# Optimization experiments

Measured on AMD Instinct MI355X. Metric: run time of the kernel, lower is better.

The kernel has to match this reference:

```python
import jax, jax.numpy as jnp
import numpy as np

SEQ_LENGTH = 256
MID_O = 800
OUT_DIM = 128

def _lstm_cell(x, h, c, Wih, Whh, bih, bhh):
    # PyTorch gate order: i, f, g, o
    gates = x @ Wih.T + h @ Whh.T + bih + bhh
    i, f, g, o = jnp.split(gates, 4, axis=-1)
    c = jax.nn.sigmoid(f) * c + jax.nn.sigmoid(i) * jnp.tanh(g)
    h = jax.nn.sigmoid(o) * jnp.tanh(c)
    return h, c

def _lstm_layer(x_seq, Wih, Whh, bih, bhh):
    B = x_seq.shape[1]
    H = Whh.shape[1]
    h0 = jnp.zeros((B, H), x_seq.dtype)
    c0 = jnp.zeros((B, H), x_seq.dtype)
    def step(carry, xt):
        h, c = carry
        h, c = _lstm_cell(xt, h, c, Wih, Whh, bih, bhh)
        return (h, c), h
    (hT, cT), out = jax.lax.scan(step, (h0, c0), x_seq)
    return out, hT, cT

def _lstm_params(key, in_dim, hid, scale=0.05):
    k1, k2, k3, k4 = jax.random.split(key, 4)
    return (jax.random.normal(k1, (4 * hid, in_dim), jnp.float32) * scale,
            jax.random.normal(k2, (4 * hid, hid), jnp.float32) * scale,
            jax.random.normal(k3, (4 * hid,), jnp.float32) * scale,
            jax.random.normal(k4, (4 * hid,), jnp.float32) * scale)

def setup_inputs() -> dict:
    key = jax.random.key(0)
    ks = jax.random.split(key, 10)
    input_dim, mid_i, latent, mid_o, out_dim = 128, 60, 20, MID_O, OUT_DIM
    x = jax.random.normal(ks[0], (SEQ_LENGTH, 1024, input_dim), jnp.float32)
    fc1 = _lstm_params(ks[1], input_dim, mid_i)
    fc21 = _lstm_params(ks[2], mid_i, latent)
    l3 = _lstm_params(ks[3], latent, latent)
    l4 = _lstm_params(ks[4], latent, mid_o)
    l5 = _lstm_params(ks[5], mid_o, out_dim)
    id_W = jax.random.normal(ks[6], (latent, latent), jnp.float32) * 0.05
    id_b = jnp.zeros((latent,), jnp.float32)
    down_W = jax.random.normal(ks[7], (latent, out_dim), jnp.float32) * 0.05
    down_b = jnp.zeros((latent,), jnp.float32)
    d = {"x": x,
         "fc1_Wih": fc1[0], "fc1_Whh": fc1[1], "fc1_bih": fc1[2], "fc1_bhh": fc1[3],
         "fc21_Wih": fc21[0], "fc21_Whh": fc21[1], "fc21_bih": fc21[2], "fc21_bhh": fc21[3],
         "l3_Wih": l3[0], "l3_Whh": l3[1], "l3_bih": l3[2], "l3_bhh": l3[3],
         "l4_Wih": l4[0], "l4_Whh": l4[1], "l4_bih": l4[2], "l4_bhh": l4[3],
         "l5_Wih": l5[0], "l5_Whh": l5[1], "l5_bih": l5[2], "l5_bhh": l5[3],
         "id_W": id_W, "id_b": id_b, "down_W": down_W, "down_b": down_b}
    return d

def reference(x, fc1_Wih, fc1_Whh, fc1_bih, fc1_bhh,
              fc21_Wih, fc21_Whh, fc21_bih, fc21_bhh,
              l3_Wih, l3_Whh, l3_bih, l3_bhh,
              l4_Wih, l4_Whh, l4_bih, l4_bhh,
              l5_Wih, l5_Whh, l5_bih, l5_bhh,
              id_W, id_b, down_W, down_b):
    # ---- encode ----
    out1, _, _ = _lstm_layer(x, fc1_Wih, fc1_Whh, fc1_bih, fc1_bhh)
    h1 = jax.nn.relu(out1)
    _, mu, c_mean = _lstm_layer(h1, fc21_Wih, fc21_Whh, fc21_bih, fc21_bhh)
    # ---- decode (deterministic: z = mu, c_t = cell_mean) ----
    B = mu.shape[0]
    output0 = mu @ id_W.T + id_b
    h2 = jnp.zeros((B, MID_O), x.dtype); c2 = jnp.zeros((B, MID_O), x.dtype)
    h3 = jnp.zeros((B, OUT_DIM), x.dtype); c3 = jnp.zeros((B, OUT_DIM), x.dtype)
    def step(carry, _):
        h, c, h2, c2, h3, c3, out = carry
        h, c = _lstm_cell(out, h, c, l3_Wih, l3_Whh, l3_bih, l3_bhh)
        h2, c2 = _lstm_cell(h, h2, c2, l4_Wih, l4_Whh, l4_bih, l4_bhh)
        h3, c3 = _lstm_cell(h2, h3, c3, l5_Wih, l5_Whh, l5_bih, l5_bhh)
        out = h3 @ down_W.T + down_b
        return (h, c, h2, c2, h3, c3, out), h3
    _, outMean = jax.lax.scan(step, (mu, c_mean, h2, c2, h3, c3, output0), None, length=SEQ_LENGTH)
    return outMean, mu
```

## Files before the change

kernel.cpp:

```cpp
#include <hip/hip_runtime.h>
#include <stdint.h>

typedef __bf16 bf16x8 __attribute__((ext_vector_type(8)));
typedef float  f32x4  __attribute__((ext_vector_type(4)));

static __device__ __forceinline__ unsigned short f2bf(float f) {
  unsigned int u = __float_as_uint(f);
  u = u + 0x7fffu + ((u >> 16) & 1u);
  return (unsigned short)(u >> 16);
}
static __device__ __forceinline__ float bf2f(unsigned short h) {
  return __uint_as_float(((unsigned int)h) << 16);
}
static __device__ __forceinline__ float sigm(float x) {
  return 1.f / (1.f + __expf(-x));
}
static __device__ __forceinline__ float tanh_f(float x) {
  float ax = fabsf(x);
  float e = __expf(-2.f * ax);
  float t = (1.f - e) / (1.f + e);
  return copysignf(t, x);
}

__global__ void kPrep(const float* __restrict__ w4i, const float* __restrict__ w4h,
                      const float* __restrict__ b4i, const float* __restrict__ b4h,
                      const float* __restrict__ w5i, const float* __restrict__ w5h,
                      const float* __restrict__ b5i, const float* __restrict__ b5h,
                      const float* __restrict__ w1i, const float* __restrict__ w1h,
                      const float* __restrict__ b1i, const float* __restrict__ b1h,
                      const float* __restrict__ w2i, const float* __restrict__ w2h,
                      const float* __restrict__ b2i, const float* __restrict__ b2h,
                      const float* __restrict__ w3i, const float* __restrict__ w3h,
                      const float* __restrict__ b3i, const float* __restrict__ b3h,
                      unsigned short* __restrict__ W4, unsigned short* __restrict__ W5,
                      float* __restrict__ W1, float* __restrict__ W2, float* __restrict__ W3,
                      float* __restrict__ b4, float* __restrict__ b5,
                      float* __restrict__ b1, float* __restrict__ b2, float* __restrict__ b3) {
  int idx0 = blockIdx.x * blockDim.x + threadIdx.x;
  int stride = gridDim.x * blockDim.x;
  const int TOT = 3197328;
  for (int i = idx0; i < TOT; i += stride) {
    int i2 = i;
    if (i2 < 2662400) {
      int n = i2 / 832, k = i2 % 832;
      float v = (k < 20) ? w4i[n * 20 + k]
                         : ((k >= 24 && k < 824) ? w4h[n * 800 + (k - 24)] : 0.f);
      W4[i2] = f2bf(v);
      continue;
    }
    i2 -= 2662400;
    if (i2 < 475136) {
      int n = i2 / 928, k = i2 % 928;
      float v = (k < 800) ? w5i[n * 800 + k] : w5h[n * 128 + (k - 800)];
      W5[i2] = f2bf(v);
      continue;
    }
    i2 -= 475136;
    if (i2 < 46080) {
      int n = i2 / 192, k = i2 % 192;
      W1[i2] = (k < 128) ? w1i[n * 128 + k] : ((k < 188) ? w1h[n * 60 + (k - 128)] : 0.f);
      continue;
    }
    i2 -= 46080;
    if (i2 < 6400) {
      int n = i2 / 80, k = i2 % 80;
      W2[i2] = (k < 60) ? w2i[n * 60 + k] : w2h[n * 20 + (k - 60)];
      continue;
    }
    i2 -= 6400;
    if (i2 < 3200) {
      int n = i2 / 40, k = i2 % 40;
      W3[i2] = (k < 20) ? w3i[n * 20 + k] : w3h[n * 20 + (k - 20)];
      continue;
    }
    i2 -= 3200;
    if (i2 < 3200) { b4[i2] = b4i[i2] + b4h[i2]; continue; }
    i2 -= 3200;
    if (i2 < 512) { b5[i2] = b5i[i2] + b5h[i2]; continue; }
    i2 -= 512;
    if (i2 < 240) { b1[i2] = b1i[i2] + b1h[i2]; continue; }
    i2 -= 240;
    if (i2 < 80) { b2[i2] = b2i[i2] + b2h[i2]; continue; }
    i2 -= 80;
    b3[i2] = b3i[i2] + b3h[i2];
  }
}

__global__ void kZero(float* __restrict__ c2, float* __restrict__ c3,
                      unsigned int* __restrict__ h2, unsigned int* __restrict__ h3) {
  int idx = blockIdx.x * blockDim.x + threadIdx.x;
  int stride = gridDim.x * blockDim.x;
  for (int i = idx; i < 819200; i += stride) c2[i] = 0.f;
  for (int i = idx; i < 131072; i += stride) c3[i] = 0.f;
  for (int i = idx; i < 409600; i += stride) h2[i] = 0u;
  for (int i = idx; i < 65536; i += stride) h3[i] = 0u;
}

__global__ __launch_bounds__(256, 2)
void kEnc(const float* __restrict__ x,
          const float* __restrict__ W1, const float* __restrict__ b1,
          const float* __restrict__ W2, const float* __restrict__ b2,
          const float* __restrict__ idW, const float* __restrict__ idb,
          float* __restrict__ hl30, float* __restrict__ cl30,
          float* __restrict__ out0, float* __restrict__ muOut) {
  __shared__ float xb[512];
  __shared__ float hb[240], cbb[240], h1b[240];
  __shared__ float h21[80], c21[80];
  __shared__ float g1[960], g2[320];
  const int tid = threadIdx.x;
  const int rowbase = blockIdx.x * 4;
  if (tid < 240) { hb[tid] = 0.f; cbb[tid] = 0.f; h1b[tid] = 0.f; }
  if (tid < 80) { h21[tid] = 0.f; c21[tid] = 0.f; }
  __syncthreads();
  for (int t = 0; t < 256; ++t) {
    const float* xs = x + ((size_t)t * 1024 + rowbase) * 128;
    xb[tid] = xs[tid];
    xb[tid + 256] = xs[tid + 256];
    __syncthreads();
    if (tid < 240) {
      const float* wr = W1 + tid * 192;
      float s0 = b1[tid], s1 = s0, s2 = s0, s3 = s0;
      for (int k = 0; k < 128; ++k) {
        float w = wr[k];
        s0 += w * xb[k]; s1 += w * xb[128 + k]; s2 += w * xb[256 + k]; s3 += w * xb[384 + k];
      }
      for (int k = 0; k < 60; ++k) {
        float w = wr[128 + k];
        s0 += w * hb[k]; s1 += w * hb[60 + k]; s2 += w * hb[120 + k]; s3 += w * hb[180 + k];
      }
      g1[tid] = s0; g1[240 + tid] = s1; g1[480 + tid] = s2; g1[720 + tid] = s3;
    }
    __syncthreads();
    if (tid < 240) {
      int b = tid / 60, j = tid % 60;
      const float* g = g1 + b * 240;
      float iv = sigm(g[j]), fv = sigm(g[60 + j]), gv = tanh_f(g[120 + j]), ov = sigm(g[180 + j]);
      float c = fv * cbb[b * 60 + j] + iv * gv;
      cbb[b * 60 + j] = c;
      float h = ov * tanh_f(c);
      hb[b * 60 + j] = h;
      h1b[b * 60 + j] = fmaxf(h, 0.f);
    }
    __syncthreads();
    if (tid < 80) {
      const float* wr = W2 + tid * 80;
      float s0 = b2[tid], s1 = s0, s2 = s0, s3 = s0;
      for (int k = 0; k < 60; ++k) {
        float w = wr[k];
        s0 += w * h1b[k]; s1 += w * h1b[60 + k]; s2 += w * h1b[120 + k]; s3 += w * h1b[180 + k];
      }
      for (int k = 0; k < 20; ++k) {
        float w = wr[60 + k];
        s0 += w * h21[k]; s1 += w * h21[20 + k]; s2 += w * h21[40 + k]; s3 += w * h21[60 + k];
      }
      g2[tid] = s0; g2[80 + tid] = s1; g2[160 + tid] = s2; g2[240 + tid] = s3;
    }
    __syncthreads();
    if (tid < 80) {
      int b = tid / 20, j = tid % 20;
      const float* g = g2 + b * 80;
      float iv = sigm(g[j]), fv = sigm(g[20 + j]), gv = tanh_f(g[40 + j]), ov = sigm(g[60 + j]);
      float c = fv * c21[b * 20 + j] + iv * gv;
      c21[b * 20 + j] = c;
      h21[b * 20 + j] = ov * tanh_f(c);
    }
    __syncthreads();
  }
  if (tid < 80) {
    int b = tid / 20, j = tid % 20;
    int gb = rowbase + b;
    float mu = h21[b * 20 + j];
    muOut[(size_t)gb * 20 + j] = mu;
    hl30[gb * 20 + j] = mu;
    cl30[gb * 20 + j] = c21[b * 20 + j];
    float s = idb[j];
    for (int k = 0; k < 20; ++k) s += h21[b * 20 + k] * idW[j * 20 + k];
    out0[gb * 20 + j] = s;
  }
}

__global__ __launch_bounds__(256, 2)
void kD1(int t,
         const unsigned short* __restrict__ W4, const float* __restrict__ b4,
         const float* __restrict__ W3, const float* __restrict__ b3,
         const float* __restrict__ dW, const float* __restrict__ db,
         const float* __restrict__ out0,
         const float* __restrict__ hl3_in, const float* __restrict__ cl3_in,
         float* __restrict__ hl3_out, float* __restrict__ cl3_out,
         const unsigned short* __restrict__ h2_in, unsigned short* __restrict__ h2_out,
         float* __restrict__ c2, const unsigned short* __restrict__ h3_in) {
  __shared__ __align__(16) unsigned short lsA[32 * 840];
  __shared__ float lsHnew[640];
  float* lsOut = (float*)lsA;
  float* lsGates = (float*)(lsA + 1280);
  unsigned short* lsH3p = lsA + 6400;

  const int tid = threadIdx.x;
  const int rowbase = blockIdx.y * 32;
  const int cb = blockIdx.x * 64;
  const int ncols = (cb + 64 <= 800) ? 64 : (800 - cb);

  if (t > 0) {
    const uint4* src = (const uint4*)(h3_in + (size_t)rowbase * 128);
    uint4* dst = (uint4*)lsH3p;
    for (int i = tid; i < 512; i += 256) dst[i] = src[i];
  }
  __syncthreads();
  if (t == 0) {
    for (int i = tid; i < 640; i += 256) {
      int b = i / 20, k = i % 20;
      lsOut[i] = out0[(size_t)(rowbase + b) * 20 + k];
    }
  } else {
    for (int i = tid; i < 640; i += 256) {
      int b = i / 20, k = i % 20;
      const float* wr = dW + k * 128;
      const unsigned short* hr = lsH3p + b * 128;
      float s = db[k];
      for (int j = 0; j < 128; ++j) s += bf2f(hr[j]) * wr[j];
      lsOut[i] = s;
    }
  }
  __syncthreads();
  for (int i = tid; i < 2560; i += 256) {
    int b = i / 80, n = i % 80;
    const float* wr = W3 + n * 40;
    const float* ob = lsOut + b * 20;
    const float* hp = hl3_in + (size_t)(rowbase + b) * 20;
    float s = b3[n];
    for (int k = 0; k < 20; ++k) s += ob[k] * wr[k];
    for (int k = 0; k < 20; ++k) s += hp[k] * wr[20 + k];
    lsGates[i] = s;
  }
  __syncthreads();
  for (int i = tid; i < 640; i += 256) {
    int b = i / 20, j = i % 20;
    const float* g = lsGates + b * 80;
    float iv = sigm(g[j]), fv = sigm(g[20 + j]), gv = tanh_f(g[40 + j]), ov = sigm(g[60 + j]);
    float c = fv * cl3_in[(size_t)(rowbase + b) * 20 + j] + iv * gv;
    float h = ov * tanh_f(c);
    lsHnew[i] = h;
    if (blockIdx.x == 0) {
      hl3_out[(size_t)(rowbase + b) * 20 + j] = h;
      cl3_out[(size_t)(rowbase + b) * 20 + j] = c;
    }
  }
  __syncthreads();
  for (int i = tid; i < 3200; i += 256) {
    int b = i / 100, s = i % 100;
    *(uint4*)(lsA + b * 840 + 24 + s * 8) =
        *(const uint4*)(h2_in + (size_t)(rowbase + b) * 800 + s * 8);
  }
  for (int i = tid; i < 640; i += 256) {
    int b = i / 20, j = i % 20;
    lsA[b * 840 + j] = f2bf(lsHnew[i]);
  }
  for (int i = tid; i < 640; i += 256) {
    int b = i / 20, z = i % 20;
    int col = (z < 4) ? (20 + z) : (820 + z);
    lsA[b * 840 + col] = 0;
  }
  __syncthreads();

  const int w = tid >> 6, lane = tid & 63, quad = lane >> 4, l16 = lane & 15;
  const int jwl = w * 16;
  if (jwl < ncols) {
    const int jw = cb + jwl;
    f32x4 acc[2][4];
#pragma unroll
    for (int mt = 0; mt < 2; ++mt)
#pragma unroll
      for (int g = 0; g < 4; ++g) acc[mt][g] = (f32x4){0.f, 0.f, 0.f, 0.f};
    const unsigned short* Wp = W4 + (size_t)(jw + l16) * 832 + quad * 8;
    const unsigned short* A0 = lsA + l16 * 840 + quad * 8;
    const unsigned short* A1 = lsA + (16 + l16) * 840 + quad * 8;
    for (int kc = 0; kc < 26; ++kc) {
      const int ko = kc * 32;
      bf16x8 a0 = *(const bf16x8*)(A0 + ko);
      bf16x8 a1 = *(const bf16x8*)(A1 + ko);
      bf16x8 bv0 = *(const bf16x8*)(Wp + (size_t)0 * 665600 + ko);
      bf16x8 bv1 = *(const bf16x8*)(Wp + (size_t)1 * 665600 + ko);
      bf16x8 bv2 = *(const bf16x8*)(Wp + (size_t)2 * 665600 + ko);
      bf16x8 bv3 = *(const bf16x8*)(Wp + (size_t)3 * 665600 + ko);
      acc[0][0] = __builtin_amdgcn_mfma_f32_16x16x32_bf16(a0, bv0, acc[0][0], 0, 0, 0);
      acc[1][0] = __builtin_amdgcn_mfma_f32_16x16x32_bf16(a1, bv0, acc[1][0], 0, 0, 0);
      acc[0][1] = __builtin_amdgcn_mfma_f32_16x16x32_bf16(a0, bv1, acc[0][1], 0, 0, 0);
      acc[1][1] = __builtin_amdgcn_mfma_f32_16x16x32_bf16(a1, bv1, acc[1][1], 0, 0, 0);
      acc[0][2] = __builtin_amdgcn_mfma_f32_16x16x32_bf16(a0, bv2, acc[0][2], 0, 0, 0);
      acc[1][2] = __builtin_amdgcn_mfma_f32_16x16x32_bf16(a1, bv2, acc[1][2], 0, 0, 0);
      acc[0][3] = __builtin_amdgcn_mfma_f32_16x16x32_bf16(a0, bv3, acc[0][3], 0, 0, 0);
      acc[1][3] = __builtin_amdgcn_mfma_f32_16x16x32_bf16(a1, bv3, acc[1][3], 0, 0, 0);
    }
    const int j = jw + l16;
    const float bi = b4[j], bff = b4[800 + j], bgg = b4[1600 + j], bo = b4[2400 + j];
#pragma unroll
    for (int mt = 0; mt < 2; ++mt) {
#pragma unroll
      for (int r = 0; r < 4; ++r) {
        int bg = rowbase + mt * 16 + quad * 4 + r;
        float iv = sigm(acc[mt][0][r] + bi);
        float fv = sigm(acc[mt][1][r] + bff);
        float gv = tanh_f(acc[mt][2][r] + bgg);
        float ov = sigm(acc[mt][3][r] + bo);
        size_t ix = (size_t)bg * 800 + j;
        float c = fv * c2[ix] + iv * gv;
        c2[ix] = c;
        h2_out[ix] = f2bf(ov * tanh_f(c));
      }
    }
  }
}

__global__ __launch_bounds__(256, 2)
void kD2(int t,
         const unsigned short* __restrict__ W5, const float* __restrict__ b5,
         const unsigned short* __restrict__ h2_cur,
         const unsigned short* __restrict__ h3_in, unsigned short* __restrict__ h3_out,
         float* __restrict__ c3, float* __restrict__ dout) {
  __shared__ __align__(16) unsigned short lsA[32 * 968];
  const int tid = threadIdx.x;
  const int rowbase = blockIdx.y * 32;
  const int colbase = blockIdx.x * 32;
  for (int i = tid; i < 3200; i += 256) {
    int b = i / 100, s = i % 100;
    *(uint4*)(lsA + b * 968 + s * 8) =
        *(const uint4*)(h2_cur + (size_t)(rowbase + b) * 800 + s * 8);
  }
  for (int i = tid; i < 512; i += 256) {
    int b = i / 16, s = i % 16;
    *(uint4*)(lsA + b * 968 + 800 + s * 8) =
        *(const uint4*)(h3_in + (size_t)(rowbase + b) * 128 + s * 8);
  }
  for (int i = tid; i < 1280; i += 256) {
    int b = i / 40, z = i % 40;
    lsA[b * 968 + 928 + z] = 0;
  }
  __syncthreads();
  const int w = tid >> 6, lane = tid & 63, quad = lane >> 4, l16 = lane & 15;
  const int mh = w >> 1, jh = w & 1;
  const int j = colbase + jh * 16 + l16;
  f32x4 acc[4];
#pragma unroll
  for (int g = 0; g < 4; ++g) acc[g] = (f32x4){0.f, 0.f, 0.f, 0.f};
  const unsigned short* Wp = W5 + (size_t)j * 928 + quad * 8;
  const unsigned short* Ap = lsA + (mh * 16 + l16) * 968 + quad * 8;
  for (int kc = 0; kc < 29; ++kc) {
    const int ko = kc * 32;
    bf16x8 a = *(const bf16x8*)(Ap + ko);
    bf16x8 bv0 = *(const bf16x8*)(Wp + (size_t)0 * 118784 + ko);
    bf16x8 bv1 = *(const bf16x8*)(Wp + (size_t)1 * 118784 + ko);
    bf16x8 bv2 = *(const bf16x8*)(Wp + (size_t)2 * 118784 + ko);
    bf16x8 bv3 = *(const bf16x8*)(Wp + (size_t)3 * 118784 + ko);
    acc[0] = __builtin_amdgcn_mfma_f32_16x16x32_bf16(a, bv0, acc[0], 0, 0, 0);
    acc[1] = __builtin_amdgcn_mfma_f32_16x16x32_bf16(a, bv1, acc[1], 0, 0, 0);
    acc[2] = __builtin_amdgcn_mfma_f32_16x16x32_bf16(a, bv2, acc[2], 0, 0, 0);
    acc[3] = __builtin_amdgcn_mfma_f32_16x16x32_bf16(a, bv3, acc[3], 0, 0, 0);
  }
  const float bi = b5[j], bff = b5[128 + j], bgg = b5[256 + j], bo = b5[384 + j];
#pragma unroll
  for (int r = 0; r < 4; ++r) {
    int bg = rowbase + mh * 16 + quad * 4 + r;
    float iv = sigm(acc[0][r] + bi);
    float fv = sigm(acc[1][r] + bff);
    float gv = tanh_f(acc[2][r] + bgg);
    float ov = sigm(acc[3][r] + bo);
    size_t ix = (size_t)bg * 128 + j;
    float c = fv * c3[ix] + iv * gv;
    c3[ix] = c;
    float h = ov * tanh_f(c);
    dout[(size_t)t * 131072 + ix] = h;
    h3_out[ix] = f2bf(h);
  }
}

extern "C" void kernel_launch(void* const* d_in, const int* in_sizes, int n_in,
                              void* d_out, int out_size, void* d_ws, size_t ws_size,
                              hipStream_t stream) {
  (void)in_sizes; (void)n_in; (void)out_size; (void)ws_size;
  const float* x   = (const float*)d_in[0];
  const float* w1i = (const float*)d_in[1];
  const float* w1h = (const float*)d_in[2];
  const float* b1i = (const float*)d_in[3];
  const float* b1h = (const float*)d_in[4];
  const float* w2i = (const float*)d_in[5];
  const float* w2h = (const float*)d_in[6];
  const float* b2i = (const float*)d_in[7];
  const float* b2h = (const float*)d_in[8];
  const float* w3i = (const float*)d_in[9];
  const float* w3h = (const float*)d_in[10];
  const float* b3i = (const float*)d_in[11];
  const float* b3h = (const float*)d_in[12];
  const float* w4i = (const float*)d_in[13];
  const float* w4h = (const float*)d_in[14];
  const float* b4i = (const float*)d_in[15];
  const float* b4h = (const float*)d_in[16];
  const float* w5i = (const float*)d_in[17];
  const float* w5h = (const float*)d_in[18];
  const float* b5i = (const float*)d_in[19];
  const float* b5h = (const float*)d_in[20];
  const float* idW = (const float*)d_in[21];
  const float* idb = (const float*)d_in[22];
  const float* dW  = (const float*)d_in[23];
  const float* db  = (const float*)d_in[24];
  float* out = (float*)d_out;

  char* ws = (char*)d_ws;
  size_t off = 0;
  auto alloc = [&](size_t bytes) -> void* {
    void* p = ws + off;
    off = (off + bytes + 255) & ~(size_t)255;
    return p;
  };
  unsigned short* W4 = (unsigned short*)alloc(3200 * 832 * 2);
  unsigned short* W5 = (unsigned short*)alloc(512 * 928 * 2);
  float* W1 = (float*)alloc(240 * 192 * 4);
  float* W2 = (float*)alloc(80 * 80 * 4);
  float* W3 = (float*)alloc(80 * 40 * 4);
  float* b4 = (float*)alloc(3200 * 4);
  float* b5 = (float*)alloc(512 * 4);
  float* b1 = (float*)alloc(240 * 4);
  float* b2 = (float*)alloc(80 * 4);
  float* b3 = (float*)alloc(80 * 4);
  unsigned short* h2buf = (unsigned short*)alloc(2 * 1024 * 800 * 2);
  unsigned short* h3buf = (unsigned short*)alloc(2 * 1024 * 128 * 2);
  float* c2 = (float*)alloc(1024 * 800 * 4);
  float* c3 = (float*)alloc(1024 * 128 * 4);
  float* hl3 = (float*)alloc(2 * 1024 * 20 * 4);
  float* cl3 = (float*)alloc(2 * 1024 * 20 * 4);
  float* out0 = (float*)alloc(1024 * 20 * 4);

  kPrep<<<dim3(4096), dim3(256), 0, stream>>>(
      w4i, w4h, b4i, b4h, w5i, w5h, b5i, b5h, w1i, w1h, b1i, b1h,
      w2i, w2h, b2i, b2h, w3i, w3h, b3i, b3h,
      W4, W5, W1, W2, W3, b4, b5, b1, b2, b3);
  kZero<<<dim3(2048), dim3(256), 0, stream>>>(c2, c3, (unsigned int*)h2buf,
                                              (unsigned int*)h3buf);
  kEnc<<<dim3(256), dim3(256), 0, stream>>>(x, W1, b1, W2, b2, idW, idb,
                                            hl3, cl3, out0, out + 33554432);

  for (int t = 0; t < 256; ++t) {
    int p = t & 1;
    const unsigned short* h2_in = h2buf + (size_t)p * 819200;
    unsigned short* h2_out = h2buf + (size_t)(1 - p) * 819200;
    const unsigned short* h3_in = h3buf + (size_t)p * 131072;
    unsigned short* h3_out = h3buf + (size_t)(1 - p) * 131072;
    const float* hl3_in = hl3 + (size_t)p * 20480;
    float* hl3_out = hl3 + (size_t)(1 - p) * 20480;
    const float* cl3_in = cl3 + (size_t)p * 20480;
    float* cl3_out = cl3 + (size_t)(1 - p) * 20480;
    kD1<<<dim3(13, 32), dim3(256), 0, stream>>>(
        t, W4, b4, W3, b3, dW, db, out0, hl3_in, cl3_in, hl3_out, cl3_out,
        h2_in, h2_out, c2, h3_in);
    kD2<<<dim3(4, 32), dim3(256), 0, stream>>>(t, W5, b5, h2_out, h3_in, h3_out,
                                               c3, out);
  }
}
```

Baseline: 22.12 ms.

## Fuse decoder time loop into one persistent kernel with grid barriers

```diff
diff --git a/kernel.cpp b/kernel.cpp
--- a/kernel.cpp
+++ b/kernel.cpp
@@ -32,7 +32,7 @@
                       const float* __restrict__ b2i, const float* __restrict__ b2h,
                       const float* __restrict__ w3i, const float* __restrict__ w3h,
                       const float* __restrict__ b3i, const float* __restrict__ b3h,
-                      unsigned short* __restrict__ W4, unsigned short* __restrict__ W5,
+                      unsigned short* __restrict__ W4F, unsigned short* __restrict__ W5,
                       float* __restrict__ W1, float* __restrict__ W2, float* __restrict__ W3,
                       float* __restrict__ b4, float* __restrict__ b5,
                       float* __restrict__ b1, float* __restrict__ b2, float* __restrict__ b3) {
@@ -42,10 +42,19 @@
   for (int i = idx0; i < TOT; i += stride) {
     int i2 = i;
     if (i2 < 2662400) {
-      int n = i2 / 832, k = i2 % 832;
-      float v = (k < 20) ? w4i[n * 20 + k]
-                         : ((k >= 24 && k < 824) ? w4h[n * 800 + (k - 24)] : 0.f);
-      W4[i2] = f2bf(v);
+      int T = i2 / 13312;
+      int r1 = i2 % 13312;
+      int kc = r1 / 512;
+      int e = r1 % 512;
+      int lane = e >> 3, j = e & 7;
+      int q = lane >> 4, l16 = lane & 15;
+      int gate = ((T & 1) ? 2 : 0) + (l16 >> 3);
+      int col = (T >> 1) * 8 + (l16 & 7);
+      int wrow = gate * 800 + col;
+      int k = kc * 32 + q * 8 + j;
+      float v = (k < 20) ? w4i[wrow * 20 + k]
+                         : ((k >= 24 && k < 824) ? w4h[wrow * 800 + (k - 24)] : 0.f);
+      W4F[i2] = f2bf(v);
       continue;
     }
     i2 -= 2662400;
@@ -86,14 +95,11 @@
   }
 }
 
-__global__ void kZero(float* __restrict__ c2, float* __restrict__ c3,
-                      unsigned int* __restrict__ h2, unsigned int* __restrict__ h3) {
+__global__ void kZero(unsigned int* __restrict__ pk, unsigned int* __restrict__ bf) {
   int idx = blockIdx.x * blockDim.x + threadIdx.x;
   int stride = gridDim.x * blockDim.x;
-  for (int i = idx; i < 819200; i += stride) c2[i] = 0.f;
-  for (int i = idx; i < 131072; i += stride) c3[i] = 0.f;
-  for (int i = idx; i < 409600; i += stride) h2[i] = 0u;
-  for (int i = idx; i < 65536; i += stride) h3[i] = 0u;
+  for (int i = idx; i < 974848; i += stride) pk[i] = 0u;
+  if (idx < 128) bf[idx] = 0u;
 }
 
 __global__ __launch_bounds__(256, 2)
@@ -179,197 +185,249 @@
   }
 }
 
-__global__ __launch_bounds__(256, 2)
-void kD1(int t,
-         const unsigned short* __restrict__ W4, const float* __restrict__ b4,
-         const float* __restrict__ W3, const float* __restrict__ b3,
-         const float* __restrict__ dW, const float* __restrict__ db,
-         const float* __restrict__ out0,
-         const float* __restrict__ hl3_in, const float* __restrict__ cl3_in,
-         float* __restrict__ hl3_out, float* __restrict__ cl3_out,
-         const unsigned short* __restrict__ h2_in, unsigned short* __restrict__ h2_out,
-         float* __restrict__ c2, const unsigned short* __restrict__ h3_in) {
-  __shared__ __align__(16) unsigned short lsA[32 * 840];
-  __shared__ float lsHnew[640];
-  float* lsOut = (float*)lsA;
-  float* lsGates = (float*)(lsA + 1280);
-  unsigned short* lsH3p = lsA + 6400;
+#define NBLK 256
+
+static __device__ __forceinline__ void gbar(unsigned int* bar, unsigned int target) {
+  __syncthreads();
+  if (threadIdx.x == 0) {
+    __hip_atomic_fetch_add(bar, 1u, __ATOMIC_RELEASE, __HIP_MEMORY_SCOPE_AGENT);
+    while (__hip_atomic_load(bar, __ATOMIC_RELAXED, __HIP_MEMORY_SCOPE_AGENT) < target)
+      __builtin_amdgcn_s_sleep(1);
+    (void)__hip_atomic_load(bar, __ATOMIC_ACQUIRE, __HIP_MEMORY_SCOPE_AGENT);
+  }
+  __syncthreads();
+}
+
+__global__ __launch_bounds__(256, 1)
+void kDec(const unsigned short* __restrict__ W4F, const float* __restrict__ b4,
+          const unsigned short* __restrict__ W5, const float* __restrict__ b5,
+          const float* __restrict__ W3g, const float* __restrict__ b3g,
+          const float* __restrict__ dWg, const float* __restrict__ dbg,
+          const float* __restrict__ out0, const float* __restrict__ hl3g,
+          const float* __restrict__ cl3g,
+          unsigned short* __restrict__ pk0, unsigned short* __restrict__ pk1,
+          float* __restrict__ dout, unsigned int* __restrict__ barflag) {
+  __shared__ __align__(16) char smem[59792];
+  unsigned int* bar = barflag;
+  unsigned int* flag = barflag + 64;
 
   const int tid = threadIdx.x;
-  const int rowbase = blockIdx.y * 32;
-  const int cb = blockIdx.x * 64;
-  const int ncols = (cb + 64 <= 800) ? 64 : (800 - cb);
-
-  if (t > 0) {
-    const uint4* src = (const uint4*)(h3_in + (size_t)rowbase * 128);
-    uint4* dst = (uint4*)lsH3p;
-    for (int i = tid; i < 512; i += 256) dst[i] = src[i];
-  }
+  const int b = blockIdx.x;
+  const int lane = tid & 63, wv = tid >> 6;
+  const int q = lane >> 4, l16 = lane & 15;
+
+  float* red = (float*)(smem + 49552);
+  float* S = (float*)smem;
+  float* lsHl = S;
+  float* lsCl = S + 640;
+  float* lsOut = S + 1280;
+  float* lsG = S + 1920;
+  float* lsW3 = S + 4480;
+  float* lsb3 = S + 7680;
+  float* lsdW = S + 7760;
+  float* lsdb = S + 10320;
+  unsigned short* lsH3 = (unsigned short*)(S + 10340);
+
+  const bool isL4 = (b < 200);
+  const bool isL3 = (b >= 200) && (b < 232);
+
+  const int cg = b % 25, rg = b / 25;
+  const int colOct = cg * 4 + wv;
+  const int col4 = colOct * 8 + (l16 & 7);
+  const bool lo = (l16 & 8) == 0;
+  bf16x8 B40[26], B41[26];
+  float bb0 = 0.f, bb1 = 0.f;
+  float c2reg[32];
+  if (isL4) {
+    const int T0 = cg * 8 + wv * 2;
+    const unsigned short* p0 = W4F + (size_t)T0 * 13312 + lane * 8;
+    const unsigned short* p1 = W4F + (size_t)(T0 + 1) * 13312 + lane * 8;
+#pragma unroll
+    for (int kc = 0; kc < 26; ++kc) {
+      B40[kc] = *(const bf16x8*)(p0 + kc * 512);
+      B41[kc] = *(const bf16x8*)(p1 + kc * 512);
+    }
+    const int g0 = (l16 >> 3), g1 = 2 + (l16 >> 3);
+    bb0 = b4[g0 * 800 + col4];
+    bb1 = b4[g1 * 800 + col4];
+#pragma unroll
+    for (int i = 0; i < 32; ++i) c2reg[i] = 0.f;
+  }
+  const int rb3 = (b - 200) * 32;
+  if (isL3) {
+    for (int i = tid; i < 3200; i += 256) lsW3[i] = W3g[i];
+    for (int i = tid; i < 2560; i += 256) lsdW[i] = dWg[i];
+    if (tid < 80) lsb3[tid] = b3g[tid];
+    if (tid < 20) lsdb[tid] = dbg[tid];
+    for (int i = tid; i < 640; i += 256) {
+      lsHl[i] = hl3g[rb3 * 20 + i];
+      lsCl[i] = cl3g[rb3 * 20 + i];
+    }
+  }
+  const int ry = b >> 3, jx = b & 7;
+  const int rowf = wv & 1, kh = wv >> 1;
+  const int rb5 = ry * 32 + rowf * 16;
+  const int u5 = jx * 16 + l16;
+  float c3reg[4] = {0.f, 0.f, 0.f, 0.f};
+  const float bi5 = b5[u5], bf5 = b5[128 + u5], bg5 = b5[256 + u5], bo5 = b5[384 + u5];
+  const size_t Aoff5 = (size_t)(rb5 + l16) * 952 + 24 + q * 8;
+  const unsigned short* Brow5[4];
+#pragma unroll
+  for (int g = 0; g < 4; ++g) Brow5[g] = W5 + (size_t)(g * 128 + u5) * 928 + q * 8;
+
   __syncthreads();
-  if (t == 0) {
-    for (int i = tid; i < 640; i += 256) {
-      int b = i / 20, k = i % 20;
-      lsOut[i] = out0[(size_t)(rowbase + b) * 20 + k];
-    }
-  } else {
-    for (int i = tid; i < 640; i += 256) {
-      int b = i / 20, k = i % 20;
-      const float* wr = dW + k * 128;
-      const unsigned short* hr = lsH3p + b * 128;
-      float s = db[k];
-      for (int j = 0; j < 128; ++j) s += bf2f(hr[j]) * wr[j];
-      lsOut[i] = s;
-    }
-  }
-  __syncthreads();
-  for (int i = tid; i < 2560; i += 256) {
-    int b = i / 80, n = i % 80;
-    const float* wr = W3 + n * 40;
-    const float* ob = lsOut + b * 20;
-    const float* hp = hl3_in + (size_t)(rowbase + b) * 20;
-    float s = b3[n];
-    for (int k = 0; k < 20; ++k) s += ob[k] * wr[k];
-    for (int k = 0; k < 20; ++k) s += hp[k] * wr[20 + k];
-    lsGates[i] = s;
-  }
-  __syncthreads();
-  for (int i = tid; i < 640; i += 256) {
-    int b = i / 20, j = i % 20;
-    const float* g = lsGates + b * 80;
-    float iv = sigm(g[j]), fv = sigm(g[20 + j]), gv = tanh_f(g[40 + j]), ov = sigm(g[60 + j]);
-    float c = fv * cl3_in[(size_t)(rowbase + b) * 20 + j] + iv * gv;
-    float h = ov * tanh_f(c);
-    lsHnew[i] = h;
-    if (blockIdx.x == 0) {
-      hl3_out[(size_t)(rowbase + b) * 20 + j] = h;
-      cl3_out[(size_t)(rowbase + b) * 20 + j] = c;
-    }
-  }
-  __syncthreads();
-  for (int i = tid; i < 3200; i += 256) {
-    int b = i / 100, s = i % 100;
-    *(uint4*)(lsA + b * 840 + 24 + s * 8) =
-        *(const uint4*)(h2_in + (size_t)(rowbase + b) * 800 + s * 8);
-  }
-  for (int i = tid; i < 640; i += 256) {
-    int b = i / 20, j = i % 20;
-    lsA[b * 840 + j] = f2bf(lsHnew[i]);
-  }
-  for (int i = tid; i < 640; i += 256) {
-    int b = i / 20, z = i % 20;
-    int col = (z < 4) ? (20 + z) : (820 + z);
-    lsA[b * 840 + col] = 0;
-  }
-  __syncthreads();
-
-  const int w = tid >> 6, lane = tid & 63, quad = lane >> 4, l16 = lane & 15;
-  const int jwl = w * 16;
-  if (jwl < ncols) {
-    const int jw = cb + jwl;
-    f32x4 acc[2][4];
-#pragma unroll
-    for (int mt = 0; mt < 2; ++mt)
-#pragma unroll
-      for (int g = 0; g < 4; ++g) acc[mt][g] = (f32x4){0.f, 0.f, 0.f, 0.f};
-    const unsigned short* Wp = W4 + (size_t)(jw + l16) * 832 + quad * 8;
-    const unsigned short* A0 = lsA + l16 * 840 + quad * 8;
-    const unsigned short* A1 = lsA + (16 + l16) * 840 + quad * 8;
-    for (int kc = 0; kc < 26; ++kc) {
-      const int ko = kc * 32;
-      bf16x8 a0 = *(const bf16x8*)(A0 + ko);
-      bf16x8 a1 = *(const bf16x8*)(A1 + ko);
-      bf16x8 bv0 = *(const bf16x8*)(Wp + (size_t)0 * 665600 + ko);
-      bf16x8 bv1 = *(const bf16x8*)(Wp + (size_t)1 * 665600 + ko);
-      bf16x8 bv2 = *(const bf16x8*)(Wp + (size_t)2 * 665600 + ko);
-      bf16x8 bv3 = *(const bf16x8*)(Wp + (size_t)3 * 665600 + ko);
-      acc[0][0] = __builtin_amdgcn_mfma_f32_16x16x32_bf16(a0, bv0, acc[0][0], 0, 0, 0);
-      acc[1][0] = __builtin_amdgcn_mfma_f32_16x16x32_bf16(a1, bv0, acc[1][0], 0, 0, 0);
-      acc[0][1] = __builtin_amdgcn_mfma_f32_16x16x32_bf16(a0, bv1, acc[0][1], 0, 0, 0);
-      acc[1][1] = __builtin_amdgcn_mfma_f32_16x16x32_bf16(a1, bv1, acc[1][1], 0, 0, 0);
-      acc[0][2] = __builtin_amdgcn_mfma_f32_16x16x32_bf16(a0, bv2, acc[0][2], 0, 0, 0);
-      acc[1][2] = __builtin_amdgcn_mfma_f32_16x16x32_bf16(a1, bv2, acc[1][2], 0, 0, 0);
-      acc[0][3] = __builtin_amdgcn_mfma_f32_16x16x32_bf16(a0, bv3, acc[0][3], 0, 0, 0);
-      acc[1][3] = __builtin_amdgcn_mfma_f32_16x16x32_bf16(a1, bv3, acc[1][3], 0, 0, 0);
-    }
-    const int j = jw + l16;
-    const float bi = b4[j], bff = b4[800 + j], bgg = b4[1600 + j], bo = b4[2400 + j];
-#pragma unroll
-    for (int mt = 0; mt < 2; ++mt) {
-#pragma unroll
-      for (int r = 0; r < 4; ++r) {
-        int bg = rowbase + mt * 16 + quad * 4 + r;
-        float iv = sigm(acc[mt][0][r] + bi);
-        float fv = sigm(acc[mt][1][r] + bff);
-        float gv = tanh_f(acc[mt][2][r] + bgg);
-        float ov = sigm(acc[mt][3][r] + bo);
-        size_t ix = (size_t)bg * 800 + j;
-        float c = fv * c2[ix] + iv * gv;
-        c2[ix] = c;
-        h2_out[ix] = f2bf(ov * tanh_f(c));
-      }
-    }
-  }
-}
-
-__global__ __launch_bounds__(256, 2)
-void kD2(int t,
-         const unsigned short* __restrict__ W5, const float* __restrict__ b5,
-         const unsigned short* __restrict__ h2_cur,
-         const unsigned short* __restrict__ h3_in, unsigned short* __restrict__ h3_out,
-         float* __restrict__ c3, float* __restrict__ dout) {
-  __shared__ __align__(16) unsigned short lsA[32 * 968];
-  const int tid = threadIdx.x;
-  const int rowbase = blockIdx.y * 32;
-  const int colbase = blockIdx.x * 32;
-  for (int i = tid; i < 3200; i += 256) {
-    int b = i / 100, s = i % 100;
-    *(uint4*)(lsA + b * 968 + s * 8) =
-        *(const uint4*)(h2_cur + (size_t)(rowbase + b) * 800 + s * 8);
-  }
-  for (int i = tid; i < 512; i += 256) {
-    int b = i / 16, s = i % 16;
-    *(uint4*)(lsA + b * 968 + 800 + s * 8) =
-        *(const uint4*)(h3_in + (size_t)(rowbase + b) * 128 + s * 8);
-  }
-  for (int i = tid; i < 1280; i += 256) {
-    int b = i / 40, z = i % 40;
-    lsA[b * 968 + 928 + z] = 0;
-  }
-  __syncthreads();
-  const int w = tid >> 6, lane = tid & 63, quad = lane >> 4, l16 = lane & 15;
-  const int mh = w >> 1, jh = w & 1;
-  const int j = colbase + jh * 16 + l16;
-  f32x4 acc[4];
-#pragma unroll
-  for (int g = 0; g < 4; ++g) acc[g] = (f32x4){0.f, 0.f, 0.f, 0.f};
-  const unsigned short* Wp = W5 + (size_t)j * 928 + quad * 8;
-  const unsigned short* Ap = lsA + (mh * 16 + l16) * 968 + quad * 8;
-  for (int kc = 0; kc < 29; ++kc) {
-    const int ko = kc * 32;
-    bf16x8 a = *(const bf16x8*)(Ap + ko);
-    bf16x8 bv0 = *(const bf16x8*)(Wp + (size_t)0 * 118784 + ko);
-    bf16x8 bv1 = *(const bf16x8*)(Wp + (size_t)1 * 118784 + ko);
-    bf16x8 bv2 = *(const bf16x8*)(Wp + (size_t)2 * 118784 + ko);
-    bf16x8 bv3 = *(const bf16x8*)(Wp + (size_t)3 * 118784 + ko);
-    acc[0] = __builtin_amdgcn_mfma_f32_16x16x32_bf16(a, bv0, acc[0], 0, 0, 0);
-    acc[1] = __builtin_amdgcn_mfma_f32_16x16x32_bf16(a, bv1, acc[1], 0, 0, 0);
-    acc[2] = __builtin_amdgcn_mfma_f32_16x16x32_bf16(a, bv2, acc[2], 0, 0, 0);
-    acc[3] = __builtin_amdgcn_mfma_f32_16x16x32_bf16(a, bv3, acc[3], 0, 0, 0);
-  }
-  const float bi = b5[j], bff = b5[128 + j], bgg = b5[256 + j], bo = b5[384 + j];
-#pragma unroll
-  for (int r = 0; r < 4; ++r) {
-    int bg = rowbase + mh * 16 + quad * 4 + r;
-    float iv = sigm(acc[0][r] + bi);
-    float fv = sigm(acc[1][r] + bff);
-    float gv = tanh_f(acc[2][r] + bgg);
-    float ov = sigm(acc[3][r] + bo);
-    size_t ix = (size_t)bg * 128 + j;
-    float c = fv * c3[ix] + iv * gv;
-    c3[ix] = c;
-    float h = ov * tanh_f(c);
-    dout[(size_t)t * 131072 + ix] = h;
-    h3_out[ix] = f2bf(h);
+
+  unsigned int barTarget = 0;
+  for (int t = 0; t < 256; ++t) {
+    unsigned short* pkR = (t & 1) ? pk1 : pk0;
+    unsigned short* pkW = (t & 1) ? pk0 : pk1;
+    if (isL3) {
+      if (t == 0) {
+        for (int i = tid; i < 640; i += 256) lsOut[i] = out0[rb3 * 20 + i];
+      } else {
+        for (int i = tid; i < 512; i += 256) {
+          int r = i >> 4, s = i & 15;
+          *(uint4*)(lsH3 + r * 128 + s * 8) =
+              *(const uint4*)(pkR + (size_t)(rb3 + r) * 952 + 824 + s * 8);
+        }
+        __syncthreads();
+        for (int i = tid; i < 640; i += 256) {
+          int r = i / 20, k = i - r * 20;
+          const unsigned short* hr = lsH3 + r * 128;
+          const float* wr = lsdW + k * 128;
+          float s = lsdb[k];
+          for (int j = 0; j < 128; ++j) s += bf2f(hr[j]) * wr[j];
+          lsOut[i] = s;
+        }
+      }
+      __syncthreads();
+      for (int i = tid; i < 2560; i += 256) {
+        int r = i / 80, n = i - r * 80;
+        const float* wr = lsW3 + n * 40;
+        const float* ob = lsOut + r * 20;
+        const float* hp = lsHl + r * 20;
+        float s = lsb3[n];
+#pragma unroll
+        for (int k = 0; k < 20; ++k) s += ob[k] * wr[k];
+#pragma unroll
+        for (int k = 0; k < 20; ++k) s += hp[k] * wr[20 + k];
+        lsG[i] = s;
+      }
+      __syncthreads();
+      for (int i = tid; i < 640; i += 256) {
+        int r = i / 20, j = i - r * 20;
+        const float* g = lsG + r * 80;
+        float cv = sigm(g[20 + j]) * lsCl[i] + sigm(g[j]) * tanh_f(g[40 + j]);
+        float hv = sigm(g[60 + j]) * tanh_f(cv);
+        lsCl[i] = cv;
+        lsHl[i] = hv;
+        pkR[(size_t)(rb3 + r) * 952 + j] = f2bf(hv);
+      }
+      __syncthreads();
+      if (tid == 0)
+        __hip_atomic_fetch_add(flag, 1u, __ATOMIC_RELEASE, __HIP_MEMORY_SCOPE_AGENT);
+    } else if (isL4) {
+      f32x4 acc[8][2];
+#pragma unroll
+      for (int mi = 0; mi < 8; ++mi) {
+        acc[mi][0] = (f32x4){0.f, 0.f, 0.f, 0.f};
+        acc[mi][1] = (f32x4){0.f, 0.f, 0.f, 0.f};
+      }
+      const unsigned short* Ab = pkR + (size_t)(rg * 128 + l16) * 952 + q * 8;
+#pragma unroll
+      for (int kc = 1; kc < 26; ++kc) {
+        bf16x8 a[8];
+#pragma unroll
+        for (int mi = 0; mi < 8; ++mi)
+          a[mi] = *(const bf16x8*)(Ab + (size_t)mi * 15232 + kc * 32);
+#pragma unroll
+        for (int mi = 0; mi < 8; ++mi) {
+          acc[mi][0] = __builtin_amdgcn_mfma_f32_16x16x32_bf16(a[mi], B40[kc], acc[mi][0], 0, 0, 0);
+          acc[mi][1] = __builtin_amdgcn_mfma_f32_16x16x32_bf16(a[mi], B41[kc], acc[mi][1], 0, 0, 0);
+        }
+      }
+      if (tid == 0) {
+        while (__hip_atomic_load(flag, __ATOMIC_RELAXED, __HIP_MEMORY_SCOPE_AGENT) < 32u * (t + 1))
+          __builtin_amdgcn_s_sleep(1);
+        (void)__hip_atomic_load(flag, __ATOMIC_ACQUIRE, __HIP_MEMORY_SCOPE_AGENT);
+      }
+      __syncthreads();
+#pragma unroll
+      for (int mi = 0; mi < 8; ++mi) {
+        bf16x8 a0 = *(const bf16x8*)(Ab + (size_t)mi * 15232);
+        acc[mi][0] = __builtin_amdgcn_mfma_f32_16x16x32_bf16(a0, B40[0], acc[mi][0], 0, 0, 0);
+        acc[mi][1] = __builtin_amdgcn_mfma_f32_16x16x32_bf16(a0, B41[0], acc[mi][1], 0, 0, 0);
+      }
+#pragma unroll
+      for (int mi = 0; mi < 8; ++mi) {
+#pragma unroll
+        for (int r = 0; r < 4; ++r) {
+          float v0 = acc[mi][0][r] + bb0;
+          float v1 = acc[mi][1][r] + bb1;
+          float p0 = __shfl_xor(v0, 8);
+          float p1 = __shfl_xor(v1, 8);
+          float iv = sigm(lo ? v0 : p0);
+          float fv = sigm(lo ? p0 : v0);
+          float gv = tanh_f(lo ? v1 : p1);
+          float ov = sigm(lo ? p1 : v1);
+          float cv = fv * c2reg[mi * 4 + r] + iv * gv;
+          c2reg[mi * 4 + r] = cv;
+          float hv = ov * tanh_f(cv);
+          if (lo)
+            pkW[(size_t)(rg * 128 + mi * 16 + q * 4 + r) * 952 + 24 + col4] = f2bf(hv);
+        }
+      }
+    }
+    barTarget += NBLK;
+    gbar(bar, barTarget);
+    {
+      f32x4 a5[4];
+#pragma unroll
+      for (int g = 0; g < 4; ++g) a5[g] = (f32x4){0.f, 0.f, 0.f, 0.f};
+      const int kcB = kh ? 15 : 0, kcE = kh ? 25 : 15;
+      for (int kc = kcB; kc < kcE; ++kc) {
+        bf16x8 av = *(const bf16x8*)(pkW + Aoff5 + kc * 32);
+#pragma unroll
+        for (int g = 0; g < 4; ++g) {
+          bf16x8 bv = *(const bf16x8*)(Brow5[g] + kc * 32);
+          a5[g] = __builtin_amdgcn_mfma_f32_16x16x32_bf16(av, bv, a5[g], 0, 0, 0);
+        }
+      }
+      if (kh) {
+        for (int kc = 25; kc < 29; ++kc) {
+          bf16x8 av = *(const bf16x8*)(pkR + Aoff5 + kc * 32);
+#pragma unroll
+          for (int g = 0; g < 4; ++g) {
+            bf16x8 bv = *(const bf16x8*)(Brow5[g] + kc * 32);
+            a5[g] = __builtin_amdgcn_mfma_f32_16x16x32_bf16(av, bv, a5[g], 0, 0, 0);
+          }
+        }
+        float* myred = red + (rowf * 64 + lane) * 20;
+#pragma unroll
+        for (int g = 0; g < 4; ++g) *(f32x4*)(myred + g * 4) = a5[g];
+      }
+      __syncthreads();
+      if (!kh) {
+        const float* myred = red + (rowf * 64 + lane) * 20;
+#pragma unroll
+        for (int g = 0; g < 4; ++g) a5[g] += *(const f32x4*)(myred + g * 4);
+#pragma unroll
+        for (int r = 0; r < 4; ++r) {
+          int row = rb5 + q * 4 + r;
+          float iv = sigm(a5[0][r] + bi5);
+          float fv = sigm(a5[1][r] + bf5);
+          float gv = tanh_f(a5[2][r] + bg5);
+          float ov = sigm(a5[3][r] + bo5);
+          float cv = fv * c3reg[r] + iv * gv;
+          c3reg[r] = cv;
+          float hv = ov * tanh_f(cv);
+          dout[(size_t)t * 131072 + (size_t)row * 128 + u5] = hv;
+          pkW[(size_t)row * 952 + 824 + u5] = f2bf(hv);
+        }
+      }
+    }
+    barTarget += NBLK;
+    if (t < 255) gbar(bar, barTarget);
   }
 }
 
@@ -400,8 +458,8 @@
   const float* b5h = (const float*)d_in[20];
   const float* idW = (const float*)d_in[21];
   const float* idb = (const float*)d_in[22];
-  const float* dW  = (const float*)d_in[23];
-  const float* db  = (const float*)d_in[24];
+  const float* dWp = (const float*)d_in[23];
+  const float* dbp = (const float*)d_in[24];
   float* out = (float*)d_out;
 
   char* ws = (char*)d_ws;
@@ -411,7 +469,7 @@
     off = (off + bytes + 255) & ~(size_t)255;
     return p;
   };
-  unsigned short* W4 = (unsigned short*)alloc(3200 * 832 * 2);
+  unsigned short* W4F = (unsigned short*)alloc(3200 * 832 * 2);
   unsigned short* W5 = (unsigned short*)alloc(512 * 928 * 2);
   float* W1 = (float*)alloc(240 * 192 * 4);
   float* W2 = (float*)alloc(80 * 80 * 4);
@@ -421,37 +479,20 @@
   float* b1 = (float*)alloc(240 * 4);
   float* b2 = (float*)alloc(80 * 4);
   float* b3 = (float*)alloc(80 * 4);
-  unsigned short* h2buf = (unsigned short*)alloc(2 * 1024 * 800 * 2);
-  unsigned short* h3buf = (unsigned short*)alloc(2 * 1024 * 128 * 2);
-  float* c2 = (float*)alloc(1024 * 800 * 4);
-  float* c3 = (float*)alloc(1024 * 128 * 4);
-  float* hl3 = (float*)alloc(2 * 1024 * 20 * 4);
-  float* cl3 = (float*)alloc(2 * 1024 * 20 * 4);
+  unsigned short* pk0 = (unsigned short*)alloc((size_t)1024 * 952 * 2);
+  unsigned short* pk1 = (unsigned short*)alloc((size_t)1024 * 952 * 2);
+  float* hl3 = (float*)alloc(1024 * 20 * 4);
+  float* cl3 = (float*)alloc(1024 * 20 * 4);
   float* out0 = (float*)alloc(1024 * 20 * 4);
+  unsigned int* barflag = (unsigned int*)alloc(512);
 
   kPrep<<<dim3(4096), dim3(256), 0, stream>>>(
       w4i, w4h, b4i, b4h, w5i, w5h, b5i, b5h, w1i, w1h, b1i, b1h,
       w2i, w2h, b2i, b2h, w3i, w3h, b3i, b3h,
-      W4, W5, W1, W2, W3, b4, b5, b1, b2, b3);
-  kZero<<<dim3(2048), dim3(256), 0, stream>>>(c2, c3, (unsigned int*)h2buf,
-                                              (unsigned int*)h3buf);
+      W4F, W5, W1, W2, W3, b4, b5, b1, b2, b3);
+  kZero<<<dim3(1024), dim3(256), 0, stream>>>((unsigned int*)pk0, barflag);
   kEnc<<<dim3(256), dim3(256), 0, stream>>>(x, W1, b1, W2, b2, idW, idb,
                                             hl3, cl3, out0, out + 33554432);
-
-  for (int t = 0; t < 256; ++t) {
-    int p = t & 1;
-    const unsigned short* h2_in = h2buf + (size_t)p * 819200;
-    unsigned short* h2_out = h2buf + (size_t)(1 - p) * 819200;
-    const unsigned short* h3_in = h3buf + (size_t)p * 131072;
-    unsigned short* h3_out = h3buf + (size_t)(1 - p) * 131072;
-    const float* hl3_in = hl3 + (size_t)p * 20480;
-    float* hl3_out = hl3 + (size_t)(1 - p) * 20480;
-    const float* cl3_in = cl3 + (size_t)p * 20480;
-    float* cl3_out = cl3 + (size_t)(1 - p) * 20480;
-    kD1<<<dim3(13, 32), dim3(256), 0, stream>>>(
-        t, W4, b4, W3, b3, dW, db, out0, hl3_in, cl3_in, hl3_out, cl3_out,
-        h2_in, h2_out, c2, h3_in);
-    kD2<<<dim3(4, 32), dim3(256), 0, stream>>>(t, W5, b5, h2_out, h3_in, h3_out,
-                                               c3, out);
-  }
-}
+  kDec<<<dim3(256), dim3(256), 0, stream>>>(W4F, b4, W5, b5, W3, b3, dWp, dbp,
+                                            out0, hl3, cl3, pk0, pk1, out, barflag);
+}
```

New measurement: 24.76 ms. 11.9% more time.
